# Optimization experiments

Hardware: AMD Instinct MI355X
Metric: run time of the kernel (lower is better)

The kernel has to match this reference:

```python
import jax, jax.numpy as jnp
import numpy as np

B, S, DM, H, HD = 2, 4096, 768, 12, 64
SCALING = HD ** -0.5
LN_EPS = 1e-12
ROPE_BASE = 10000.0


def rotate_half(x):
    x1, x2 = jnp.split(x, 2, axis=-1)
    return jnp.concatenate([-x2, x1], axis=-1)


def setup_inputs() -> dict:
    key = jax.random.key(0)
    ks = jax.random.split(key, 8)
    s = 0.02
    hidden_states = jax.random.normal(ks[0], (B, S, DM), dtype=jnp.float32)
    # true rotary tables: inv_freq over head_dim/2, duplicated (HF convention)
    inv_freq = 1.0 / (ROPE_BASE ** (jnp.arange(0, HD, 2, dtype=jnp.float32) / HD))
    freqs = jnp.arange(S, dtype=jnp.float32)[:, None] * inv_freq[None, :]  # [S, HD/2]
    emb = jnp.concatenate([freqs, freqs], axis=-1)                          # [S, HD]
    cos, sin = jnp.cos(emb), jnp.sin(emb)
    return {
        "hidden_states": hidden_states,
        "cos": cos,
        "sin": sin,
        "Wq": jax.random.normal(ks[1], (DM, DM), dtype=jnp.float32) * s,
        "bq": jnp.zeros((DM,), dtype=jnp.float32),
        "Wk": jax.random.normal(ks[2], (DM, DM), dtype=jnp.float32) * s,
        "bk": jnp.zeros((DM,), dtype=jnp.float32),
        "Wv": jax.random.normal(ks[3], (DM, DM), dtype=jnp.float32) * s,
        "bv": jnp.zeros((DM,), dtype=jnp.float32),
        "Wo": jax.random.normal(ks[4], (DM, DM), dtype=jnp.float32) * s,
        "ln_g": jnp.ones((DM,), dtype=jnp.float32),
        "ln_b": jnp.zeros((DM,), dtype=jnp.float32),
    }


def reference(hidden_states, cos, sin, Wq, bq, Wk, bk, Wv, bv, Wo, ln_g, ln_b):
    # QKV projections -> [B, H, S, HD]
    def proj(W, b):
        return (hidden_states @ W.T + b).reshape(B, S, H, HD).transpose(0, 2, 1, 3)
    q, k, v = proj(Wq, bq), proj(Wk, bk), proj(Wv, bv)

    # RoPE (cos/sin broadcast over batch & heads)
    c = cos[None, None, :, :]
    s_ = sin[None, None, :, :]
    q = q * c + rotate_half(q) * s_
    k = k * c + rotate_half(k) * s_

    # Faithful to source: q pre-scaled, then eager attention scales scores again
    q = q * SCALING
    scores = jnp.einsum("bhsd,bhtd->bhst", q, k) * SCALING  # [B,H,S,S]
    probs = jax.nn.softmax(scores.astype(jnp.float32), axis=-1).astype(v.dtype)
    attn = jnp.einsum("bhst,bhtd->bhsd", probs, v)
    attn = attn.transpose(0, 2, 1, 3).reshape(B, S, DM)

    # output dense (no bias) + residual + LayerNorm
    out = attn @ Wo.T + hidden_states
    mu = jnp.mean(out, axis=-1, keepdims=True)
    var = jnp.var(out, axis=-1, keepdims=True)
    out = (out - mu) * jax.lax.rsqrt(var + LN_EPS) * ln_g + ln_b
    return out
```

## Files before the change

kernel.cpp:

```cpp
#include <hip/hip_runtime.h>
#include <math.h>

#define B_   2
#define S_   4096
#define DM_  768
#define H_   12
#define HD_  64
#define M_   (B_ * S_)
#define ROWELEMS ((size_t)M_ * DM_)
#define WELEMS  ((size_t)DM_ * DM_)

#define QSC (1.4426950408889634f / 64.0f)

typedef unsigned short u16;
typedef unsigned int   u32;
typedef __attribute__((ext_vector_type(8))) short  short8;
typedef __attribute__((ext_vector_type(4))) float  floatx4;

__device__ inline u16 f2bf(float f) {
    u32 u = __builtin_bit_cast(u32, f);
    u += 0x7FFF + ((u >> 16) & 1);
    return (u16)(u >> 16);
}
__device__ inline float bf2f(u16 h) {
    return __builtin_bit_cast(float, (u32)h << 16);
}
__device__ inline u32 pk_trunc(float a, float b) {
    return __builtin_amdgcn_perm(__builtin_bit_cast(u32, b),
                                 __builtin_bit_cast(u32, a), 0x07060302);
}

__device__ inline int sw_off(int r, int cg) {
    return (r << 6) + ((cg ^ (r & 7)) << 3);
}

__device__ __forceinline__ void load_lds16(const u16* g, u16* l) {
    __builtin_amdgcn_global_load_lds(
        (const __attribute__((address_space(1))) u32*)g,
        (__attribute__((address_space(3))) u32*)l, 16, 0, 0);
}

__device__ __forceinline__ void drain_vm() {
    __builtin_amdgcn_s_waitcnt(0x0F70);
}

__global__ __launch_bounds__(256) void conv_bf16(
    const float* __restrict__ h,  const float* __restrict__ wq,
    const float* __restrict__ wk, const float* __restrict__ wv,
    const float* __restrict__ wo, u16* __restrict__ hb, u16* __restrict__ wb)
{
    const int y = blockIdx.y;
    const float* src; u16* dst; size_t n4;
    if (y == 0)      { src = h;  dst = hb;              n4 = ROWELEMS / 4; }
    else if (y == 1) { src = wq; dst = wb;              n4 = WELEMS / 4; }
    else if (y == 2) { src = wk; dst = wb + WELEMS;     n4 = WELEMS / 4; }
    else if (y == 3) { src = wv; dst = wb + 2 * WELEMS; n4 = WELEMS / 4; }
    else             { src = wo; dst = wb + 3 * WELEMS; n4 = WELEMS / 4; }
    const size_t stride = (size_t)gridDim.x * 256;
    for (size_t i = blockIdx.x * 256 + threadIdx.x; i < n4; i += stride) {
        float4 v = *(const float4*)&src[i * 4];
        u32 p0 = (u32)f2bf(v.x) | ((u32)f2bf(v.y) << 16);
        u32 p1 = (u32)f2bf(v.z) | ((u32)f2bf(v.w) << 16);
        *(uint2*)&dst[i * 4] = make_uint2(p0, p1);
    }
}

__global__ __launch_bounds__(256, 3) void gemm_qkv(
    const u16* __restrict__ A,
    const u16* __restrict__ W0, const u16* __restrict__ W1, const u16* __restrict__ W2,
    const float* __restrict__ b0, const float* __restrict__ b1, const float* __restrict__ b2,
    const float* __restrict__ cosT, const float* __restrict__ sinT,
    u16* __restrict__ Qh, u16* __restrict__ Kh, u16* __restrict__ Vt)
{
    __shared__ __align__(16) u16 As[128 * 64];
    __shared__ __align__(16) u16 Ws[128 * 64];

    const int tid  = threadIdx.x;
    const int wave = tid >> 6, lane = tid & 63;
    const int n16  = lane & 15, quad = lane >> 4;
    const int wm   = wave >> 1, wn = wave & 1;
    const int m0   = blockIdx.y * 128, n0 = blockIdx.x * 128;
    const int z    = blockIdx.z;

    const u16* Wz = (z == 0) ? W0 : (z == 1) ? W1 : W2;
    const float* bz = (z == 0) ? b0 : (z == 1) ? b1 : b2;

    int gao[4], ldso[4];
#pragma unroll
    for (int i = 0; i < 4; i++) {
        int g = wave * 256 + i * 64 + lane;
        int r = g >> 3, cg = (g & 7) ^ (r & 7);
        gao[i]  = r * DM_ + cg * 8;
        ldso[i] = (wave * 256 + i * 64) * 8;
    }
    const u16* Ap = A  + (size_t)m0 * DM_;
    const u16* Wp = Wz + (size_t)n0 * DM_;

    floatx4 acc[4][4];
#pragma unroll
    for (int i = 0; i < 4; i++)
#pragma unroll
        for (int j = 0; j < 4; j++) acc[i][j] = (floatx4){0.f, 0.f, 0.f, 0.f};

    for (int k0 = 0; k0 < DM_; k0 += 64) {
        __syncthreads();
#pragma unroll
        for (int i = 0; i < 4; i++) {
            load_lds16(Ap + k0 + gao[i], &As[ldso[i]]);
            load_lds16(Wp + k0 + gao[i], &Ws[ldso[i]]);
        }
        drain_vm();
        __syncthreads();
#pragma unroll
        for (int ks = 0; ks < 2; ks++) {
            short8 af[4], bf[4];
#pragma unroll
            for (int t = 0; t < 4; t++) {
                af[t] = *(const short8*)&As[sw_off(wm * 64 + t * 16 + n16, ks * 4 + quad)];
                bf[t] = *(const short8*)&Ws[sw_off(wn * 64 + t * 16 + n16, ks * 4 + quad)];
            }
#pragma unroll
            for (int i = 0; i < 4; i++)
#pragma unroll
                for (int j = 0; j < 4; j++)
                    acc[i][j] = __builtin_amdgcn_mfma_f32_16x16x32_bf16(
                        af[i], bf[j], acc[i][j], 0, 0, 0);
        }
    }

    if (z == 2) {
#pragma unroll
        for (int i = 0; i < 4; i++)
#pragma unroll
            for (int j = 0; j < 4; j++) {
                const int col = n0 + wn * 64 + j * 16 + n16;
                const int h = col >> 6, hd = col & 63;
                const int row0 = m0 + wm * 64 + i * 16 + quad * 4;
                const int b = row0 >> 12, s0 = row0 & 4095;
                const float bias = bz[col];
                float v0 = acc[i][j][0] + bias, v1 = acc[i][j][1] + bias;
                float v2 = acc[i][j][2] + bias, v3 = acc[i][j][3] + bias;
                u32 w0 = (u32)f2bf(v0) | ((u32)f2bf(v1) << 16);
                u32 w1 = (u32)f2bf(v2) | ((u32)f2bf(v3) << 16);
                *(uint2*)&Vt[((size_t)(b * H_ + h) * HD_ + hd) * S_ + s0] = make_uint2(w0, w1);
            }
    } else {
        u32* Out32 = (u32*)((z == 0) ? Qh : Kh);
        const float sc_ = (z == 0) ? QSC : 1.0f;
#pragma unroll
        for (int i = 0; i < 4; i++)
#pragma unroll
            for (int j = 0; j < 2; j++) {
                const int col1 = n0 + wn * 64 + j * 16 + n16;
                const int col2 = col1 + 32;
                const int h = col1 >> 6, hd1 = col1 & 63;
                const float bias1 = bz[col1], bias2 = bz[col2];
#pragma unroll
                for (int r = 0; r < 4; r++) {
                    const int row = m0 + wm * 64 + i * 16 + quad * 4 + r;
                    const int b = row >> 12, s = row & 4095;
                    const float c  = cosT[s * HD_ + hd1];
                    const float sn = sinT[s * HD_ + hd1];
                    const float x1 = acc[i][j][r] + bias1;
                    const float x2 = acc[i][j + 2][r] + bias2;
                    const float y1 = (x1 * c - x2 * sn) * sc_;
                    const float y2 = (x2 * c + x1 * sn) * sc_;
                    Out32[(((size_t)(b * H_ + h) * S_ + s) << 5) + hd1] =
                        (u32)f2bf(y1) | ((u32)f2bf(y2) << 16);
                }
            }
    }
}

__global__ __launch_bounds__(256, 4) void flash_mfma(
    const u16* __restrict__ Qh, const u16* __restrict__ Kh,
    const u16* __restrict__ Vt, u16* __restrict__ O1, u16* __restrict__ O2,
    float* __restrict__ l1, float* __restrict__ l2)
{
    __shared__ __align__(16) u16 Ks[64 * 64];
    __shared__ __align__(16) u16 Vs[64 * 64];
    __shared__ __align__(16) u16 Ps[128 * 64];

    const int tid  = threadIdx.x;
    const int wave = tid >> 6, lane = tid & 63;
    const int n16  = lane & 15, quad = lane >> 4;
    const int qt   = blockIdx.x;
    const int bh   = blockIdx.y;
    const int z    = blockIdx.z;
    const size_t qk_base = (size_t)bh * S_ * HD_;
    const size_t vt_base = (size_t)bh * HD_ * S_;
    const int q0   = qt * 128;
    const int wrow = wave * 32;

    short8 qf[2][2];
#pragma unroll
    for (int rt = 0; rt < 2; rt++)
#pragma unroll
        for (int ks = 0; ks < 2; ks++)
            qf[rt][ks] = *(const short8*)&Qh[qk_base +
                (size_t)(q0 + wrow + rt * 16 + n16) * HD_ + ks * 32 + quad * 8];

    int gk_off[2], gv_off[2], ldso[2];
#pragma unroll
    for (int i = 0; i < 2; i++) {
        int g = wave * 128 + i * 64 + lane;
        int r = g >> 3, cg = (g & 7) ^ (r & 7);
        gk_off[i] = r * HD_ + cg * 8;
        gv_off[i] = r * S_  + cg * 8;
        ldso[i]   = (wave * 128 + i * 64) * 8;
    }

    floatx4 o_acc[2][4];
    float l_part[2] = {0.0f, 0.0f};
#pragma unroll
    for (int rt = 0; rt < 2; rt++)
#pragma unroll
        for (int dt = 0; dt < 4; dt++) o_acc[rt][dt] = (floatx4){0.f, 0.f, 0.f, 0.f};

    const u16* Kg = Kh + qk_base + (size_t)(z * 32) * 64 * HD_;
    const u16* Vg = Vt + vt_base + (size_t)(z * 32) * 64;

    for (int kt = 0; kt < 32; kt++) {
        __syncthreads();
#pragma unroll
        for (int i = 0; i < 2; i++) {
            load_lds16(Kg + gk_off[i], &Ks[ldso[i]]);
            load_lds16(Vg + gv_off[i], &Vs[ldso[i]]);
        }
        drain_vm();
        __syncthreads();
        Kg += 64 * HD_;
        Vg += 64;

        floatx4 sct[4][2];
#pragma unroll
        for (int ct = 0; ct < 4; ct++)
#pragma unroll
            for (int rt = 0; rt < 2; rt++)
                sct[ct][rt] = (floatx4){0.f, 0.f, 0.f, 0.f};
#pragma unroll
        for (int ks = 0; ks < 2; ks++) {
            short8 kf[4];
#pragma unroll
            for (int ct = 0; ct < 4; ct++)
                kf[ct] = *(const short8*)&Ks[sw_off(ct * 16 + n16, ks * 4 + quad)];
#pragma unroll
            for (int ct = 0; ct < 4; ct++)
#pragma unroll
                for (int rt = 0; rt < 2; rt++)
                    sct[ct][rt] = __builtin_amdgcn_mfma_f32_16x16x32_bf16(
                        kf[ct], qf[rt][ks], sct[ct][rt], 0, 0, 0);
        }

#pragma unroll
        for (int rt = 0; rt < 2; rt++)
#pragma unroll
            for (int ct = 0; ct < 4; ct++) {
                float p0 = __builtin_amdgcn_exp2f(sct[ct][rt][0]);
                float p1 = __builtin_amdgcn_exp2f(sct[ct][rt][1]);
                float p2 = __builtin_amdgcn_exp2f(sct[ct][rt][2]);
                float p3 = __builtin_amdgcn_exp2f(sct[ct][rt][3]);
                l_part[rt] += (p0 + p1) + (p2 + p3);
                uint2 w = make_uint2(pk_trunc(p0, p1), pk_trunc(p2, p3));
                const int row = wrow + rt * 16 + n16;
                const int off = sw_off(row, ct * 2 + (quad >> 1)) + (quad & 1) * 4;
                *(uint2*)&Ps[off] = w;
            }

#pragma unroll
        for (int ks = 0; ks < 2; ks++) {
            short8 pa[2];
#pragma unroll
            for (int rt = 0; rt < 2; rt++)
                pa[rt] = *(const short8*)&Ps[sw_off(wrow + rt * 16 + n16, ks * 4 + quad)];
            short8 vb[4];
#pragma unroll
            for (int dt = 0; dt < 4; dt++)
                vb[dt] = *(const short8*)&Vs[sw_off(dt * 16 + n16, ks * 4 + quad)];
#pragma unroll
            for (int rt = 0; rt < 2; rt++)
#pragma unroll
                for (int dt = 0; dt < 4; dt++)
                    o_acc[rt][dt] = __builtin_amdgcn_mfma_f32_16x16x32_bf16(
                        pa[rt], vb[dt], o_acc[rt][dt], 0, 0, 0);
        }
    }

    float* lz = z ? l2 : l1;
#pragma unroll
    for (int rt = 0; rt < 2; rt++) {
        float v = l_part[rt];
        v += __shfl_xor(v, 16);
        v += __shfl_xor(v, 32);
        if (lane < 16)
            lz[(size_t)bh * S_ + q0 + wrow + rt * 16 + lane] = v;
    }
    const int b = bh / H_, h = bh % H_;
    u16* Oz = z ? O2 : O1;
#pragma unroll
    for (int rt = 0; rt < 2; rt++)
#pragma unroll
        for (int r = 0; r < 4; r++) {
            const int srow = q0 + wrow + rt * 16 + quad * 4 + r;
            u16* Orow = Oz + ((size_t)b * S_ + srow) * DM_ + h * HD_;
#pragma unroll
            for (int dt = 0; dt < 4; dt++)
                Orow[dt * 16 + n16] = f2bf(o_acc[rt][dt][r]);
        }
}

__global__ __launch_bounds__(256, 4) void gemm_out(
    const u16* __restrict__ O1, const u16* __restrict__ O2,
    const float* __restrict__ l1, const float* __restrict__ l2,
    const u16* __restrict__ W, const float* __restrict__ resid,
    float* __restrict__ Cf)
{
    __shared__ __align__(16) u16 As[64 * 64];
    __shared__ __align__(16) u16 Ws[128 * 64];

    const int tid  = threadIdx.x;
    const int wave = tid >> 6, lane = tid & 63;
    const int n16  = lane & 15, quad = lane >> 4;
    const int wm   = wave >> 1, wn = wave & 1;
    const int m0   = blockIdx.y * 64, n0 = blockIdx.x * 128;

    int gwo[4], ldswo[4];
#pragma unroll
    for (int i = 0; i < 4; i++) {
        int g = wave * 256 + i * 64 + lane;
        int r = g >> 3, cg = (g & 7) ^ (r & 7);
        gwo[i]   = r * DM_ + cg * 8;
        ldswo[i] = (wave * 256 + i * 64) * 8;
    }
    const u16* Wp = W + (size_t)n0 * DM_;

    floatx4 acc[2][4];
#pragma unroll
    for (int i = 0; i < 2; i++)
#pragma unroll
        for (int j = 0; j < 4; j++) acc[i][j] = (floatx4){0.f, 0.f, 0.f, 0.f};

    for (int k0 = 0; k0 < DM_; k0 += 64) {
        __syncthreads();
#pragma unroll
        for (int i = 0; i < 4; i++)
            load_lds16(Wp + k0 + gwo[i], &Ws[ldswo[i]]);

#pragma unroll
        for (int i = 0; i < 2; i++) {
            const int ga = tid + i * 256;
            const int ra = ga >> 3, cga = ga & 7;
            const int row = m0 + ra;
            const int col0 = k0 + cga * 8;
            const int b = row >> 12, s = row & 4095, h = col0 >> 6;
            const size_t lidx = ((size_t)(b * H_ + h)) * S_ + s;
            const float inv = __builtin_amdgcn_rcpf(l1[lidx] + l2[lidx]);
            const size_t go = (size_t)row * DM_ + col0;
            uint4 a = *(const uint4*)&O1[go];
            uint4 c = *(const uint4*)&O2[go];
            u32 res[4];
#pragma unroll
            for (int w = 0; w < 4; w++) {
                u32 ua = (&a.x)[w], uc = (&c.x)[w];
                float x0 = bf2f((u16)(ua & 0xFFFF)) + bf2f((u16)(uc & 0xFFFF));
                float x1 = bf2f((u16)(ua >> 16))    + bf2f((u16)(uc >> 16));
                res[w] = (u32)f2bf(x0 * inv) | ((u32)f2bf(x1 * inv) << 16);
            }
            *(uint4*)&As[sw_off(ra, cga)] = make_uint4(res[0], res[1], res[2], res[3]);
        }
        drain_vm();
        __syncthreads();

#pragma unroll
        for (int ks = 0; ks < 2; ks++) {
            short8 af[2], bf[4];
#pragma unroll
            for (int rt = 0; rt < 2; rt++)
                af[rt] = *(const short8*)&As[sw_off(wm * 32 + rt * 16 + n16, ks * 4 + quad)];
#pragma unroll
            for (int ct = 0; ct < 4; ct++)
                bf[ct] = *(const short8*)&Ws[sw_off(wn * 64 + ct * 16 + n16, ks * 4 + quad)];
#pragma unroll
            for (int rt = 0; rt < 2; rt++)
#pragma unroll
                for (int ct = 0; ct < 4; ct++)
                    acc[rt][ct] = __builtin_amdgcn_mfma_f32_16x16x32_bf16(
                        af[rt], bf[ct], acc[rt][ct], 0, 0, 0);
        }
    }

#pragma unroll
    for (int rt = 0; rt < 2; rt++)
#pragma unroll
        for (int ct = 0; ct < 4; ct++) {
            const int col = n0 + wn * 64 + ct * 16 + n16;
#pragma unroll
            for (int r = 0; r < 4; r++) {
                const int row = m0 + wm * 32 + rt * 16 + quad * 4 + r;
                Cf[(size_t)row * DM_ + col] = acc[rt][ct][r] + resid[(size_t)row * DM_ + col];
            }
        }
}

__global__ __launch_bounds__(256) void ln_kernel(
    float* __restrict__ io, const float* __restrict__ g, const float* __restrict__ bb)
{
    const int row = blockIdx.x, t = threadIdx.x;
    float* p = io + (size_t)row * DM_;
    float x[3];
    float sum = 0.0f, sq = 0.0f;
#pragma unroll
    for (int i = 0; i < 3; i++) {
        x[i] = p[t + i * 256];
        sum += x[i];
        sq  = fmaf(x[i], x[i], sq);
    }
#pragma unroll
    for (int off = 32; off >= 1; off >>= 1) {
        sum += __shfl_xor(sum, off);
        sq  += __shfl_xor(sq, off);
    }
    __shared__ float s1[4], s2[4];
    if ((t & 63) == 0) { s1[t >> 6] = sum; s2[t >> 6] = sq; }
    __syncthreads();
    sum = s1[0] + s1[1] + s1[2] + s1[3];
    sq  = s2[0] + s2[1] + s2[2] + s2[3];
    const float mu  = sum * (1.0f / 768.0f);
    const float var = sq * (1.0f / 768.0f) - mu * mu;
    const float rs  = rsqrtf(var + 1e-12f);
#pragma unroll
    for (int i = 0; i < 3; i++) {
        const int c = t + i * 256;
        p[c] = (x[i] - mu) * rs * g[c] + bb[c];
    }
}

extern "C" void kernel_launch(void* const* d_in, const int* in_sizes, int n_in,
                              void* d_out, int out_size, void* d_ws, size_t ws_size,
                              hipStream_t stream)
{
    const float* hidden = (const float*)d_in[0];
    const float* cosT   = (const float*)d_in[1];
    const float* sinT   = (const float*)d_in[2];
    const float* Wq     = (const float*)d_in[3];
    const float* bq     = (const float*)d_in[4];
    const float* Wk     = (const float*)d_in[5];
    const float* bk     = (const float*)d_in[6];
    const float* Wv     = (const float*)d_in[7];
    const float* bv     = (const float*)d_in[8];
    const float* Wo     = (const float*)d_in[9];
    const float* ln_g   = (const float*)d_in[10];
    const float* ln_b   = (const float*)d_in[11];
    float* out = (float*)d_out;

    u16* wsb = (u16*)d_ws;
    u16* Hb  = wsb;
    u16* Wb  = wsb + ROWELEMS;
    u16* Qh  = Wb + 4 * WELEMS;
    u16* Kh  = Qh + ROWELEMS;
    u16* Vt  = Kh + ROWELEMS;
    u16* O2  = Vt + ROWELEMS;
    float* l1 = (float*)(O2 + ROWELEMS);
    float* l2 = l1 + (size_t)B_ * H_ * S_;
    u16* O1  = Hb;
    u16* Wqb = Wb, *Wkb = Wb + WELEMS, *Wvb = Wb + 2 * WELEMS, *Wob = Wb + 3 * WELEMS;

    conv_bf16<<<dim3(1024, 5), 256, 0, stream>>>(hidden, Wq, Wk, Wv, Wo, Hb, Wb);

    gemm_qkv<<<dim3(DM_ / 128, M_ / 128, 3), 256, 0, stream>>>(
        Hb, Wqb, Wkb, Wvb, bq, bk, bv, cosT, sinT, Qh, Kh, Vt);

    flash_mfma<<<dim3(S_ / 128, B_ * H_, 2), 256, 0, stream>>>(
        Qh, Kh, Vt, O1, O2, l1, l2);

    gemm_out<<<dim3(DM_ / 128, M_ / 64), 256, 0, stream>>>(
        O1, O2, l1, l2, Wob, hidden, out);

    ln_kernel<<<M_, 256, 0, stream>>>(out, ln_g, ln_b);
}
```

Measured before the change: 294.5 us.

## Drop split-KV in flash attention, compute row sums via MFMA, normalize in-kernel

```diff
diff --git a/kernel.cpp b/kernel.cpp
--- a/kernel.cpp
+++ b/kernel.cpp
@@ -174,8 +174,7 @@
 
 __global__ __launch_bounds__(256, 4) void flash_mfma(
     const u16* __restrict__ Qh, const u16* __restrict__ Kh,
-    const u16* __restrict__ Vt, u16* __restrict__ O1, u16* __restrict__ O2,
-    float* __restrict__ l1, float* __restrict__ l2)
+    const u16* __restrict__ Vt, u16* __restrict__ O)
 {
     __shared__ __align__(16) u16 Ks[64 * 64];
     __shared__ __align__(16) u16 Vs[64 * 64];
@@ -186,7 +185,6 @@
     const int n16  = lane & 15, quad = lane >> 4;
     const int qt   = blockIdx.x;
     const int bh   = blockIdx.y;
-    const int z    = blockIdx.z;
     const size_t qk_base = (size_t)bh * S_ * HD_;
     const size_t vt_base = (size_t)bh * HD_ * S_;
     const int q0   = qt * 128;
@@ -199,6 +197,10 @@
         for (int ks = 0; ks < 2; ks++)
             qf[rt][ks] = *(const short8*)&Qh[qk_base +
                 (size_t)(q0 + wrow + rt * 16 + n16) * HD_ + ks * 32 + quad * 8];
+
+    short8 ones;
+#pragma unroll
+    for (int j = 0; j < 8; j++) ones[j] = (short)0x3F80;
 
     int gk_off[2], gv_off[2], ldso[2];
 #pragma unroll
@@ -211,16 +213,18 @@
     }
 
     floatx4 o_acc[2][4];
-    float l_part[2] = {0.0f, 0.0f};
-#pragma unroll
-    for (int rt = 0; rt < 2; rt++)
+    floatx4 o_l[2];
+#pragma unroll
+    for (int rt = 0; rt < 2; rt++) {
+        o_l[rt] = (floatx4){0.f, 0.f, 0.f, 0.f};
 #pragma unroll
         for (int dt = 0; dt < 4; dt++) o_acc[rt][dt] = (floatx4){0.f, 0.f, 0.f, 0.f};
-
-    const u16* Kg = Kh + qk_base + (size_t)(z * 32) * 64 * HD_;
-    const u16* Vg = Vt + vt_base + (size_t)(z * 32) * 64;
-
-    for (int kt = 0; kt < 32; kt++) {
+    }
+
+    const u16* Kg = Kh + qk_base;
+    const u16* Vg = Vt + vt_base;
+
+    for (int kt = 0; kt < 64; kt++) {
         __syncthreads();
 #pragma unroll
         for (int i = 0; i < 2; i++) {
@@ -260,7 +264,6 @@
                 float p1 = __builtin_amdgcn_exp2f(sct[ct][rt][1]);
                 float p2 = __builtin_amdgcn_exp2f(sct[ct][rt][2]);
                 float p3 = __builtin_amdgcn_exp2f(sct[ct][rt][3]);
-                l_part[rt] += (p0 + p1) + (p2 + p3);
                 uint2 w = make_uint2(pk_trunc(p0, p1), pk_trunc(p2, p3));
                 const int row = wrow + rt * 16 + n16;
                 const int off = sw_off(row, ct * 2 + (quad >> 1)) + (quad & 1) * 4;
@@ -278,42 +281,34 @@
             for (int dt = 0; dt < 4; dt++)
                 vb[dt] = *(const short8*)&Vs[sw_off(dt * 16 + n16, ks * 4 + quad)];
 #pragma unroll
-            for (int rt = 0; rt < 2; rt++)
+            for (int rt = 0; rt < 2; rt++) {
 #pragma unroll
                 for (int dt = 0; dt < 4; dt++)
                     o_acc[rt][dt] = __builtin_amdgcn_mfma_f32_16x16x32_bf16(
                         pa[rt], vb[dt], o_acc[rt][dt], 0, 0, 0);
-        }
-    }
-
-    float* lz = z ? l2 : l1;
-#pragma unroll
-    for (int rt = 0; rt < 2; rt++) {
-        float v = l_part[rt];
-        v += __shfl_xor(v, 16);
-        v += __shfl_xor(v, 32);
-        if (lane < 16)
-            lz[(size_t)bh * S_ + q0 + wrow + rt * 16 + lane] = v;
-    }
+                o_l[rt] = __builtin_amdgcn_mfma_f32_16x16x32_bf16(
+                    pa[rt], ones, o_l[rt], 0, 0, 0);
+            }
+        }
+    }
+
     const int b = bh / H_, h = bh % H_;
-    u16* Oz = z ? O2 : O1;
 #pragma unroll
     for (int rt = 0; rt < 2; rt++)
 #pragma unroll
         for (int r = 0; r < 4; r++) {
+            const float inv = 1.0f / o_l[rt][r];
             const int srow = q0 + wrow + rt * 16 + quad * 4 + r;
-            u16* Orow = Oz + ((size_t)b * S_ + srow) * DM_ + h * HD_;
+            u16* Orow = O + ((size_t)b * S_ + srow) * DM_ + h * HD_;
 #pragma unroll
             for (int dt = 0; dt < 4; dt++)
-                Orow[dt * 16 + n16] = f2bf(o_acc[rt][dt][r]);
+                Orow[dt * 16 + n16] = f2bf(o_acc[rt][dt][r] * inv);
         }
 }
 
 __global__ __launch_bounds__(256, 4) void gemm_out(
-    const u16* __restrict__ O1, const u16* __restrict__ O2,
-    const float* __restrict__ l1, const float* __restrict__ l2,
-    const u16* __restrict__ W, const float* __restrict__ resid,
-    float* __restrict__ Cf)
+    const u16* __restrict__ A, const u16* __restrict__ W,
+    const float* __restrict__ resid, float* __restrict__ Cf)
 {
     __shared__ __align__(16) u16 As[64 * 64];
     __shared__ __align__(16) u16 Ws[128 * 64];
@@ -324,7 +319,7 @@
     const int wm   = wave >> 1, wn = wave & 1;
     const int m0   = blockIdx.y * 64, n0 = blockIdx.x * 128;
 
-    int gwo[4], ldswo[4];
+    int gwo[4], ldswo[4], gao[2], ldsao[2];
 #pragma unroll
     for (int i = 0; i < 4; i++) {
         int g = wave * 256 + i * 64 + lane;
@@ -332,7 +327,15 @@
         gwo[i]   = r * DM_ + cg * 8;
         ldswo[i] = (wave * 256 + i * 64) * 8;
     }
+#pragma unroll
+    for (int i = 0; i < 2; i++) {
+        int g = wave * 128 + i * 64 + lane;
+        int r = g >> 3, cg = (g & 7) ^ (r & 7);
+        gao[i]   = r * DM_ + cg * 8;
+        ldsao[i] = (wave * 128 + i * 64) * 8;
+    }
     const u16* Wp = W + (size_t)n0 * DM_;
+    const u16* Ap = A + (size_t)m0 * DM_;
 
     floatx4 acc[2][4];
 #pragma unroll
@@ -345,29 +348,9 @@
 #pragma unroll
         for (int i = 0; i < 4; i++)
             load_lds16(Wp + k0 + gwo[i], &Ws[ldswo[i]]);
-
-#pragma unroll
-        for (int i = 0; i < 2; i++) {
-            const int ga = tid + i * 256;
-            const int ra = ga >> 3, cga = ga & 7;
-            const int row = m0 + ra;
-            const int col0 = k0 + cga * 8;
-            const int b = row >> 12, s = row & 4095, h = col0 >> 6;
-            const size_t lidx = ((size_t)(b * H_ + h)) * S_ + s;
-            const float inv = __builtin_amdgcn_rcpf(l1[lidx] + l2[lidx]);
-            const size_t go = (size_t)row * DM_ + col0;
-            uint4 a = *(const uint4*)&O1[go];
-            uint4 c = *(const uint4*)&O2[go];
-            u32 res[4];
-#pragma unroll
-            for (int w = 0; w < 4; w++) {
-                u32 ua = (&a.x)[w], uc = (&c.x)[w];
-                float x0 = bf2f((u16)(ua & 0xFFFF)) + bf2f((u16)(uc & 0xFFFF));
-                float x1 = bf2f((u16)(ua >> 16))    + bf2f((u16)(uc >> 16));
-                res[w] = (u32)f2bf(x0 * inv) | ((u32)f2bf(x1 * inv) << 16);
-            }
-            *(uint4*)&As[sw_off(ra, cga)] = make_uint4(res[0], res[1], res[2], res[3]);
-        }
+#pragma unroll
+        for (int i = 0; i < 2; i++)
+            load_lds16(Ap + k0 + gao[i], &As[ldsao[i]]);
         drain_vm();
         __syncthreads();
 
@@ -459,10 +442,7 @@
     u16* Qh  = Wb + 4 * WELEMS;
     u16* Kh  = Qh + ROWELEMS;
     u16* Vt  = Kh + ROWELEMS;
-    u16* O2  = Vt + ROWELEMS;
-    float* l1 = (float*)(O2 + ROWELEMS);
-    float* l2 = l1 + (size_t)B_ * H_ * S_;
-    u16* O1  = Hb;
+    u16* Ob  = Hb;
     u16* Wqb = Wb, *Wkb = Wb + WELEMS, *Wvb = Wb + 2 * WELEMS, *Wob = Wb + 3 * WELEMS;
 
     conv_bf16<<<dim3(1024, 5), 256, 0, stream>>>(hidden, Wq, Wk, Wv, Wo, Hb, Wb);
@@ -470,11 +450,9 @@
     gemm_qkv<<<dim3(DM_ / 128, M_ / 128, 3), 256, 0, stream>>>(
         Hb, Wqb, Wkb, Wvb, bq, bk, bv, cosT, sinT, Qh, Kh, Vt);
 
-    flash_mfma<<<dim3(S_ / 128, B_ * H_, 2), 256, 0, stream>>>(
-        Qh, Kh, Vt, O1, O2, l1, l2);
-
-    gemm_out<<<dim3(DM_ / 128, M_ / 64), 256, 0, stream>>>(
-        O1, O2, l1, l2, Wob, hidden, out);
+    flash_mfma<<<dim3(S_ / 128, B_ * H_), 256, 0, stream>>>(Qh, Kh, Vt, Ob);
+
+    gemm_out<<<dim3(DM_ / 128, M_ / 64), 256, 0, stream>>>(Ob, Wob, hidden, out);
 
     ln_kernel<<<M_, 256, 0, stream>>>(out, ln_g, ln_b);
 }
```

After: 278.5 us. -5.4%, faster.
